# Kernel optimization log

Hardware: AMD Instinct MI355X
Metric: run time of the kernel (lower is better)

The kernel has to match this reference:

```python
import jax, jax.numpy as jnp
import numpy as np

SEQ, D_IN, D_OUT = 4096, 1024, 1024


def setup_inputs() -> dict:
    key = jax.random.key(0)
    k_emb, k_q, k_k, k_v = jax.random.split(key, 4)
    # torch Linear stores weight as [out, in]; we keep [in, out] for x @ W
    scale = 1.0 / np.sqrt(D_IN)
    return {
        "embeddings": jax.random.normal(k_emb, (SEQ, D_IN), dtype=jnp.float32),
        "w_query": jax.random.uniform(k_q, (D_IN, D_OUT), dtype=jnp.float32, minval=-scale, maxval=scale),
        "w_key": jax.random.uniform(k_k, (D_IN, D_OUT), dtype=jnp.float32, minval=-scale, maxval=scale),
        "w_value": jax.random.uniform(k_v, (D_IN, D_OUT), dtype=jnp.float32, minval=-scale, maxval=scale),
    }


def reference(embeddings, w_query, w_key, w_value):
    # QKV projections (bias=False)
    q = embeddings @ w_query  # [S, D_out]
    k = embeddings @ w_key    # [S, D_out]
    v = embeddings @ w_value  # [S, D_out]
    inv_sqrt_d = 1.0 / jnp.sqrt(jnp.asarray(k.shape[-1], dtype=q.dtype))
    scores = jnp.einsum("sd,td->st", q, k) * inv_sqrt_d  # [S, S]
    weights = jax.nn.softmax(scores, axis=-1)
    return weights @ v  # [S, D_out]
```

## Files before the change

kernel.cpp:

```cpp
#include <hip/hip_runtime.h>
#include <hip/hip_bf16.h>

typedef unsigned short u16;
typedef __bf16 bf16x8 __attribute__((ext_vector_type(8)));
typedef float f32x4 __attribute__((ext_vector_type(4)));
typedef unsigned short u16x8 __attribute__((ext_vector_type(8)));
typedef unsigned short u16x4 __attribute__((ext_vector_type(4)));

__device__ __forceinline__ float bf2f(u16 u) {
  unsigned x = ((unsigned)u) << 16;
  return __builtin_bit_cast(float, x);
}
__device__ __forceinline__ u16 f2bf(float f) {
  unsigned u = __builtin_bit_cast(unsigned, f);
  u += 0x7fffu + ((u >> 16) & 1u);
  return (u16)(u >> 16);
}

__device__ __forceinline__ void gload16(const u16* g, u16* lds) {
  __builtin_amdgcn_global_load_lds(
      (const __attribute__((address_space(1))) void*)g,
      (__attribute__((address_space(3))) void*)lds,
      16, 0, 0);
}

__device__ __forceinline__ void bar() {
  __builtin_amdgcn_sched_barrier(0);
  __builtin_amdgcn_s_barrier();
  __builtin_amdgcn_sched_barrier(0);
}
template <int N> __device__ __forceinline__ void wait_vm() {
  asm volatile("s_waitcnt vmcnt(%0)" :: "n"(N) : "memory");
  __builtin_amdgcn_sched_barrier(0);
}
__device__ __forceinline__ void wait_lgkm0() {
  asm volatile("s_waitcnt lgkmcnt(0)" ::: "memory");
  __builtin_amdgcn_sched_barrier(0);
}

#define OFF_A(d,h) (((d)*2+(h))*8192)
#define OFF_B(d,h) (32768 + ((d)*2+(h))*8192)

struct G256 {
  const u16 *gA0, *gA1, *gB0, *gB1;
  int dst0, dst1;
  int aoff0[4], aoff1[4], boff[4];
  u16* lds;
};

__device__ __forceinline__ int swz_slot(int row, int q) {
  return row * 4 + (q ^ ((row ^ (row >> 2)) & 3));
}

template <int W0, int W1, bool S0, bool S1>
__device__ __forceinline__ void ktile256(const G256& g, int s, f32x4 (&acc)[8][4]) {
  const int d = s & 1;
  const int kN1 = (s + 1) * 64 + 32;
  const int kN0 = (s + 2) * 64;
  bf16x8 af[8], bf[4];

#pragma unroll
  for (int i = 0; i < 4; ++i) af[i]     = *(const bf16x8*)(g.lds + OFF_A(d, 0) + g.aoff0[i]);
#pragma unroll
  for (int i = 0; i < 4; ++i) af[4 + i] = *(const bf16x8*)(g.lds + OFF_A(d, 0) + g.aoff1[i]);
#pragma unroll
  for (int j = 0; j < 4; ++j) bf[j]     = *(const bf16x8*)(g.lds + OFF_B(d, 0) + g.boff[j]);
  if (S0) {
    gload16(g.gA0 + kN1, g.lds + OFF_A(d ^ 1, 1) + g.dst0);
    gload16(g.gA1 + kN1, g.lds + OFF_A(d ^ 1, 1) + g.dst1);
    gload16(g.gB0 + kN1, g.lds + OFF_B(d ^ 1, 1) + g.dst0);
    gload16(g.gB1 + kN1, g.lds + OFF_B(d ^ 1, 1) + g.dst1);
  }
  wait_vm<W0>();
  bar();
  wait_lgkm0();
  __builtin_amdgcn_s_setprio(1);
#pragma unroll
  for (int i = 0; i < 8; ++i)
#pragma unroll
    for (int j = 0; j < 4; ++j)
      acc[i][j] = __builtin_amdgcn_mfma_f32_16x16x32_bf16(af[i], bf[j], acc[i][j], 0, 0, 0);
  __builtin_amdgcn_s_setprio(0);
  bar();

#pragma unroll
  for (int i = 0; i < 4; ++i) af[i]     = *(const bf16x8*)(g.lds + OFF_A(d, 1) + g.aoff0[i]);
#pragma unroll
  for (int i = 0; i < 4; ++i) af[4 + i] = *(const bf16x8*)(g.lds + OFF_A(d, 1) + g.aoff1[i]);
#pragma unroll
  for (int j = 0; j < 4; ++j) bf[j]     = *(const bf16x8*)(g.lds + OFF_B(d, 1) + g.boff[j]);
  if (S1) {
    gload16(g.gA0 + kN0, g.lds + OFF_A(d, 0) + g.dst0);
    gload16(g.gA1 + kN0, g.lds + OFF_A(d, 0) + g.dst1);
    gload16(g.gB0 + kN0, g.lds + OFF_B(d, 0) + g.dst0);
    gload16(g.gB1 + kN0, g.lds + OFF_B(d, 0) + g.dst1);
  }
  wait_vm<W1>();
  bar();
  wait_lgkm0();
  __builtin_amdgcn_s_setprio(1);
#pragma unroll
  for (int i = 0; i < 8; ++i)
#pragma unroll
    for (int j = 0; j < 4; ++j)
      acc[i][j] = __builtin_amdgcn_mfma_f32_16x16x32_bf16(af[i], bf[j], acc[i][j], 0, 0, 0);
  __builtin_amdgcn_s_setprio(0);
  bar();
}

template <int OUT_MODE, int NX, int NT>
__device__ __forceinline__ void gemm256_body(
    const u16* __restrict__ A, int lda, const u16* __restrict__ B, int ldb,
    void* __restrict__ C, int ldc, float cscale, u16* lds, int bid)
{
  static_assert(NT >= 3, "tail peel needs NT>=3");
  const int by = (bid & 7) + 8 * (bid / (8 * NX));
  const int bx = (bid >> 3) % NX;
  const int m0 = by * 256, n0 = bx * 256;
  const int t = threadIdx.x;
  const int w = t >> 6, l = t & 63;
  const int wm = (w >> 2) * 128, wn = (w & 3) * 64;
  const int fr = l & 15, q = l >> 4;

  G256 g;
  g.lds = lds;
  {
    const int s0 = w * 64 + l;
    const int r0 = s0 >> 2, r1 = r0 + 128;
    const int q0 = (s0 & 3) ^ ((r0 ^ (r0 >> 2)) & 3);
    const int q1 = (s0 & 3) ^ ((r1 ^ (r1 >> 2)) & 3);
    g.gA0 = A + (size_t)(m0 + r0) * lda + q0 * 8;
    g.gA1 = A + (size_t)(m0 + r1) * lda + q1 * 8;
    g.gB0 = B + (size_t)(n0 + r0) * ldb + q0 * 8;
    g.gB1 = B + (size_t)(n0 + r1) * ldb + q1 * 8;
    g.dst0 = (w * 64) * 8;
    g.dst1 = (512 + w * 64) * 8;
  }
#pragma unroll
  for (int i = 0; i < 4; ++i) {
    g.aoff0[i] = swz_slot(wm + 16 * i + fr, q) * 8;
    g.aoff1[i] = swz_slot(wm + 64 + 16 * i + fr, q) * 8;
    g.boff[i]  = swz_slot(wn + 16 * i + fr, q) * 8;
  }

  f32x4 acc[8][4] = {};

  gload16(g.gA0 + 0,  lds + OFF_A(0, 0) + g.dst0);
  gload16(g.gA1 + 0,  lds + OFF_A(0, 0) + g.dst1);
  gload16(g.gB0 + 0,  lds + OFF_B(0, 0) + g.dst0);
  gload16(g.gB1 + 0,  lds + OFF_B(0, 0) + g.dst1);
  gload16(g.gA0 + 32, lds + OFF_A(0, 1) + g.dst0);
  gload16(g.gA1 + 32, lds + OFF_A(0, 1) + g.dst1);
  gload16(g.gB0 + 32, lds + OFF_B(0, 1) + g.dst0);
  gload16(g.gB1 + 32, lds + OFF_B(0, 1) + g.dst1);
  gload16(g.gA0 + 64, lds + OFF_A(1, 0) + g.dst0);
  gload16(g.gA1 + 64, lds + OFF_A(1, 0) + g.dst1);
  gload16(g.gB0 + 64, lds + OFF_B(1, 0) + g.dst0);
  gload16(g.gB1 + 64, lds + OFF_B(1, 0) + g.dst1);
  wait_vm<8>();
  bar();

  for (int s = 0; s + 2 < NT; ++s)
    ktile256<8, 8, true, true>(g, s, acc);
  ktile256<8, 4, true, false>(g, NT - 2, acc);
  ktile256<0, 0, false, false>(g, NT - 1, acc);

  const int er = q * 4, ec = fr;
  const int rg = l >> 3, c = l & 7;

  if (OUT_MODE == 1) {
    u16* Ch = (u16*)C;
    u16* eb = lds + w * 4608;
#pragma unroll
    for (int half = 0; half < 2; ++half) {
#pragma unroll
      for (int i = 0; i < 4; ++i)
#pragma unroll
        for (int j = 0; j < 4; ++j)
#pragma unroll
          for (int r = 0; r < 4; ++r)
            eb[(16 * i + er + r) * 72 + 16 * j + ec] = f2bf(acc[4 * half + i][j][r] * cscale);
#pragma unroll
      for (int k = 0; k < 8; ++k) {
        const int row = k * 8 + rg;
        u16x8 v = *(const u16x8*)(eb + row * 72 + c * 8);
        *(u16x8*)(Ch + (size_t)(m0 + wm + 64 * half + row) * ldc + n0 + wn + c * 8) = v;
      }
    }
  } else {
    float* Cf = (float*)C;
    float* eb = (float*)lds + w * 2304;
#pragma unroll
    for (int half = 0; half < 2; ++half)
#pragma unroll
      for (int ip = 0; ip < 2; ++ip) {
#pragma unroll
        for (int ii = 0; ii < 2; ++ii)
#pragma unroll
          for (int j = 0; j < 4; ++j)
#pragma unroll
            for (int r = 0; r < 4; ++r)
              eb[(16 * ii + er + r) * 72 + 16 * j + ec] = acc[4 * half + 2 * ip + ii][j][r] * cscale;
#pragma unroll
        for (int k = 0; k < 4; ++k) {
          const int row = k * 8 + rg;
          float4 v0 = *(const float4*)(eb + row * 72 + c * 4);
          float4 v1 = *(const float4*)(eb + row * 72 + (c + 8) * 4);
          float* dst = Cf + (size_t)(m0 + wm + 64 * half + 32 * ip + row) * ldc + n0 + wn;
          *(float4*)(dst + c * 4) = v0;
          *(float4*)(dst + (c + 8) * 4) = v1;
        }
      }
  }
}

__global__ __launch_bounds__(512, 2) void gemm_qkv256(const u16* __restrict__ A,
                                                      const u16* __restrict__ B,
                                                      u16* __restrict__ C) {
  __shared__ __align__(16) u16 lds[65536];
  gemm256_body<1, 12, 16>(A, 1024, B, 1024, C, 3072, 1.0f, lds, blockIdx.x);
}

__global__ __launch_bounds__(512, 2) void gemm_score256(const u16* __restrict__ QKV,
                                                        u16* __restrict__ S) {
  __shared__ __align__(16) u16 lds[65536];
  gemm256_body<1, 16, 16>(QKV, 3072, QKV + 1024, 3072, S, 4096, 0.03125f, lds, blockIdx.x);
}

__global__ __launch_bounds__(512, 2) void gemm_pv256f(const u16* __restrict__ S,
                                                      const u16* __restrict__ Vt,
                                                      float* __restrict__ P4) {
  __shared__ __align__(16) u16 lds[65536];
  const int b = blockIdx.x;
  const int sp = b >> 6;
  float* Cp = P4 + (size_t)sp * 4096 * 1024;
  gemm256_body<0, 4, 16>(S + sp * 1024, 4096, Vt + sp * 1024, 4096,
                         Cp, 1024, 1.0f, lds, b & 63);
}

__global__ __launch_bounds__(512, 2) void gemm_pv256h(const u16* __restrict__ S,
                                                      const u16* __restrict__ Vt,
                                                      u16* __restrict__ P4) {
  __shared__ __align__(16) u16 lds[65536];
  const int b = blockIdx.x;
  const int sp = b >> 6;
  u16* Cp = P4 + (size_t)sp * 4096 * 1024;
  gemm256_body<1, 4, 16>(S + sp * 1024, 4096, Vt + sp * 1024, 4096,
                         Cp, 1024, 1.0f, lds, b & 63);
}

__global__ __launch_bounds__(256) void reduce4f(const float* __restrict__ P4,
                                                float* __restrict__ O) {
  const size_t i = ((size_t)blockIdx.x * 256 + threadIdx.x) * 4;
  const size_t st = (size_t)4096 * 1024;
  float4 a = *(const float4*)(P4 + i);
  float4 b = *(const float4*)(P4 + st + i);
  float4 c = *(const float4*)(P4 + 2 * st + i);
  float4 d = *(const float4*)(P4 + 3 * st + i);
  float4 o;
  o.x = (a.x + b.x) + (c.x + d.x);
  o.y = (a.y + b.y) + (c.y + d.y);
  o.z = (a.z + b.z) + (c.z + d.z);
  o.w = (a.w + b.w) + (c.w + d.w);
  *(float4*)(O + i) = o;
}

__global__ __launch_bounds__(256) void reduce4h(const u16* __restrict__ P4,
                                                float* __restrict__ O) {
  const size_t i = ((size_t)blockIdx.x * 256 + threadIdx.x) * 4;
  const size_t st = (size_t)4096 * 1024;
  u16x4 a = *(const u16x4*)(P4 + i);
  u16x4 b = *(const u16x4*)(P4 + st + i);
  u16x4 c = *(const u16x4*)(P4 + 2 * st + i);
  u16x4 d = *(const u16x4*)(P4 + 3 * st + i);
  float4 o;
  o.x = (bf2f(a.x) + bf2f(b.x)) + (bf2f(c.x) + bf2f(d.x));
  o.y = (bf2f(a.y) + bf2f(b.y)) + (bf2f(c.y) + bf2f(d.y));
  o.z = (bf2f(a.z) + bf2f(b.z)) + (bf2f(c.z) + bf2f(d.z));
  o.w = (bf2f(a.w) + bf2f(b.w)) + (bf2f(c.w) + bf2f(d.w));
  *(float4*)(O + i) = o;
}

__global__ __launch_bounds__(256) void prep(
    const float* __restrict__ E,
    const float* __restrict__ w0, const float* __restrict__ w1,
    const float* __restrict__ w2,
    u16* __restrict__ Ebf, u16* __restrict__ Wt)
{
  int b = blockIdx.x;
  if (b < 4096) {
    const int i = (b * 256 + threadIdx.x) * 4;
    float4 f = *(const float4*)(E + i);
    u16x4 o;
    o.x = f2bf(f.x); o.y = f2bf(f.y); o.z = f2bf(f.z); o.w = f2bf(f.w);
    *(u16x4*)(Ebf + i) = o;
  } else {
    b -= 4096;
    const int which = b >> 10;
    const int tile = b & 1023;
    const float* in = (which == 0) ? w0 : (which == 1) ? w1 : w2;
    u16* o = Wt + (size_t)which * 1024 * 1024;
    const int c0 = (tile & 31) * 32, r0 = (tile >> 5) * 32;
    __shared__ u16 tl[32][33];
    const int tx = threadIdx.x & 31, ty0 = threadIdx.x >> 5;
#pragma unroll
    for (int k = 0; k < 4; ++k) {
      const int ty = ty0 + k * 8;
      tl[ty][tx] = f2bf(in[(size_t)(r0 + ty) * 1024 + c0 + tx]);
    }
    __syncthreads();
#pragma unroll
    for (int k = 0; k < 4; ++k) {
      const int ty = ty0 + k * 8;
      o[(size_t)(c0 + ty) * 1024 + r0 + tx] = tl[tx][ty];
    }
  }
}

__global__ __launch_bounds__(256) void softmax_tv(u16* __restrict__ S,
                                                  const u16* __restrict__ QKV,
                                                  u16* __restrict__ Vt) {
  __shared__ float red[8];
  __shared__ u16 tl[32][33];
  const int b = blockIdx.x;
  if (b < 4096) {
    const int N = 4096;
    u16* p = S + (size_t)b * N;
    const int t = threadIdx.x;
    u16x8 u0 = ((const u16x8*)p)[t * 2];
    u16x8 u1 = ((const u16x8*)p)[t * 2 + 1];
    float v[16];
#pragma unroll
    for (int i = 0; i < 8; ++i) v[i] = bf2f(u0[i]);
#pragma unroll
    for (int i = 0; i < 8; ++i) v[8 + i] = bf2f(u1[i]);

    float m = -1e30f;
#pragma unroll
    for (int i = 0; i < 16; ++i) m = fmaxf(m, v[i]);
#pragma unroll
    for (int off = 32; off; off >>= 1) m = fmaxf(m, __shfl_xor(m, off));
    if ((t & 63) == 0) red[t >> 6] = m;
    __syncthreads();
    m = fmaxf(fmaxf(red[0], red[1]), fmaxf(red[2], red[3]));

    float s = 0.f;
#pragma unroll
    for (int i = 0; i < 16; ++i) { v[i] = __expf(v[i] - m); s += v[i]; }
#pragma unroll
    for (int off = 32; off; off >>= 1) s += __shfl_xor(s, off);
    if ((t & 63) == 0) red[4 + (t >> 6)] = s;
    __syncthreads();
    s = (red[4] + red[5]) + (red[6] + red[7]);
    const float inv = 1.0f / s;

    u16x8 o0, o1;
#pragma unroll
    for (int i = 0; i < 8; ++i) o0[i] = f2bf(v[i] * inv);
#pragma unroll
    for (int i = 0; i < 8; ++i) o1[i] = f2bf(v[8 + i] * inv);
    ((u16x8*)p)[t * 2] = o0;
    ((u16x8*)p)[t * 2 + 1] = o1;
  } else {
    const int v = b - 4096;
    const int c0 = (v & 31) * 32;
    const int r0 = (v >> 5) * 32;
    const int tx = threadIdx.x & 31, ty0 = threadIdx.x >> 5;
    const u16* Vin = QKV + 2048;
#pragma unroll
    for (int k = 0; k < 4; ++k) {
      const int ty = ty0 + k * 8;
      tl[ty][tx] = Vin[(size_t)(r0 + ty) * 3072 + c0 + tx];
    }
    __syncthreads();
#pragma unroll
    for (int k = 0; k < 4; ++k) {
      const int ty = ty0 + k * 8;
      Vt[(size_t)(c0 + ty) * 4096 + r0 + tx] = tl[tx][ty];
    }
  }
}

extern "C" void kernel_launch(void* const* d_in, const int* in_sizes, int n_in,
                              void* d_out, int out_size, void* d_ws, size_t ws_size,
                              hipStream_t stream) {
  const float* E  = (const float*)d_in[0];
  const float* Wq = (const float*)d_in[1];
  const float* Wk = (const float*)d_in[2];
  const float* Wv = (const float*)d_in[3];
  float* Out = (float*)d_out;

  char* w = (char*)d_ws;
  u16* Ebf = (u16*)(w);
  u16* Wt  = (u16*)(w + (size_t)(8u << 20));
  u16* QKV = (u16*)(w + (size_t)(14u << 20));
  u16* Vt  = (u16*)(w + (size_t)(38u << 20));
  u16* S   = (u16*)(w + (size_t)(46u << 20));

  prep<<<7168, 256, 0, stream>>>(E, Wq, Wk, Wv, Ebf, Wt);

  gemm_qkv256<<<192, 512, 0, stream>>>(Ebf, Wt, QKV);

  gemm_score256<<<256, 512, 0, stream>>>(QKV, S);

  softmax_tv<<<8192, 256, 0, stream>>>(S, QKV, Vt);

  if (ws_size >= ((size_t)146u << 20)) {
    float* P4 = (float*)(w + ((size_t)78u << 20));
    gemm_pv256f<<<256, 512, 0, stream>>>(S, Vt, P4);
    reduce4f<<<4096, 256, 0, stream>>>(P4, Out);
  } else {
    u16* P4 = (u16*)w;
    gemm_pv256h<<<256, 512, 0, stream>>>(S, Vt, P4);
    reduce4h<<<4096, 256, 0, stream>>>(P4, Out);
  }
}
```

Before: 218.8 us.

## Shrink GEMM tiles to 128x256 with triple-buffered K=32 pipeline

Replaces the 256x256 GEMM tile and its double-buffered two-half K pipeline with a 128x256 tile using a three-stage rotating LDS buffer at K=32 granularity and one barrier per phase. LDS per block drops, so launch bounds allow four blocks per CU, and grid sizes double to 384/512. The aim is more parallelism and better CU coverage on a 256-CU part, at the cost of lower arithmetic intensity per tile (more global/LDS traffic for the B operand) and more barriers per unit of work.

After: 221.4 us. No clear change (+1.2%).

```diff
diff --git a/kernel.cpp b/kernel.cpp
--- a/kernel.cpp
+++ b/kernel.cpp
@@ -38,133 +38,97 @@
   __builtin_amdgcn_sched_barrier(0);
 }
 
-#define OFF_A(d,h) (((d)*2+(h))*8192)
-#define OFF_B(d,h) (32768 + ((d)*2+(h))*8192)
-
-struct G256 {
-  const u16 *gA0, *gA1, *gB0, *gB1;
+__device__ __forceinline__ int h4(int r) { return ((r >> 1) ^ (r >> 3)) & 3; }
+
+#define ABUF(p) ((p) * 4096)
+#define BBUF(p) (12288 + (p) * 8192)
+
+struct GS {
+  const u16 *gA, *gB0, *gB1;
   int dst0, dst1;
-  int aoff0[4], aoff1[4], boff[4];
+  int aoff[4], boff[4];
   u16* lds;
 };
 
-__device__ __forceinline__ int swz_slot(int row, int q) {
-  return row * 4 + (q ^ ((row ^ (row >> 2)) & 3));
-}
-
-template <int W0, int W1, bool S0, bool S1>
-__device__ __forceinline__ void ktile256(const G256& g, int s, f32x4 (&acc)[8][4]) {
-  const int d = s & 1;
-  const int kN1 = (s + 1) * 64 + 32;
-  const int kN0 = (s + 2) * 64;
-  bf16x8 af[8], bf[4];
-
-#pragma unroll
-  for (int i = 0; i < 4; ++i) af[i]     = *(const bf16x8*)(g.lds + OFF_A(d, 0) + g.aoff0[i]);
-#pragma unroll
-  for (int i = 0; i < 4; ++i) af[4 + i] = *(const bf16x8*)(g.lds + OFF_A(d, 0) + g.aoff1[i]);
-#pragma unroll
-  for (int j = 0; j < 4; ++j) bf[j]     = *(const bf16x8*)(g.lds + OFF_B(d, 0) + g.boff[j]);
-  if (S0) {
-    gload16(g.gA0 + kN1, g.lds + OFF_A(d ^ 1, 1) + g.dst0);
-    gload16(g.gA1 + kN1, g.lds + OFF_A(d ^ 1, 1) + g.dst1);
-    gload16(g.gB0 + kN1, g.lds + OFF_B(d ^ 1, 1) + g.dst0);
-    gload16(g.gB1 + kN1, g.lds + OFF_B(d ^ 1, 1) + g.dst1);
-  }
-  wait_vm<W0>();
+template <bool STG, int W>
+__device__ __forceinline__ void phase128(const GS& g, int s, int p, f32x4 (&acc)[4][4]) {
+  wait_vm<W>();
   bar();
+  bf16x8 a[4], b[4];
+#pragma unroll
+  for (int i = 0; i < 4; ++i) a[i] = *(const bf16x8*)(g.lds + ABUF(p) + g.aoff[i]);
+#pragma unroll
+  for (int j = 0; j < 4; ++j) b[j] = *(const bf16x8*)(g.lds + BBUF(p) + g.boff[j]);
+  if (STG) {
+    const int kt = (s + 2) * 32;
+    const int p2 = (p + 2) % 3;
+    gload16(g.gA + kt, g.lds + ABUF(p2) + g.dst0);
+    gload16(g.gB0 + kt, g.lds + BBUF(p2) + g.dst0);
+    gload16(g.gB1 + kt, g.lds + BBUF(p2) + g.dst1);
+  }
   wait_lgkm0();
   __builtin_amdgcn_s_setprio(1);
 #pragma unroll
-  for (int i = 0; i < 8; ++i)
+  for (int i = 0; i < 4; ++i)
 #pragma unroll
     for (int j = 0; j < 4; ++j)
-      acc[i][j] = __builtin_amdgcn_mfma_f32_16x16x32_bf16(af[i], bf[j], acc[i][j], 0, 0, 0);
+      acc[i][j] = __builtin_amdgcn_mfma_f32_16x16x32_bf16(a[i], b[j], acc[i][j], 0, 0, 0);
   __builtin_amdgcn_s_setprio(0);
-  bar();
-
-#pragma unroll
-  for (int i = 0; i < 4; ++i) af[i]     = *(const bf16x8*)(g.lds + OFF_A(d, 1) + g.aoff0[i]);
-#pragma unroll
-  for (int i = 0; i < 4; ++i) af[4 + i] = *(const bf16x8*)(g.lds + OFF_A(d, 1) + g.aoff1[i]);
-#pragma unroll
-  for (int j = 0; j < 4; ++j) bf[j]     = *(const bf16x8*)(g.lds + OFF_B(d, 1) + g.boff[j]);
-  if (S1) {
-    gload16(g.gA0 + kN0, g.lds + OFF_A(d, 0) + g.dst0);
-    gload16(g.gA1 + kN0, g.lds + OFF_A(d, 0) + g.dst1);
-    gload16(g.gB0 + kN0, g.lds + OFF_B(d, 0) + g.dst0);
-    gload16(g.gB1 + kN0, g.lds + OFF_B(d, 0) + g.dst1);
-  }
-  wait_vm<W1>();
-  bar();
-  wait_lgkm0();
-  __builtin_amdgcn_s_setprio(1);
-#pragma unroll
-  for (int i = 0; i < 8; ++i)
-#pragma unroll
-    for (int j = 0; j < 4; ++j)
-      acc[i][j] = __builtin_amdgcn_mfma_f32_16x16x32_bf16(af[i], bf[j], acc[i][j], 0, 0, 0);
-  __builtin_amdgcn_s_setprio(0);
-  bar();
 }
 
 template <int OUT_MODE, int NX, int NT>
-__device__ __forceinline__ void gemm256_body(
+__device__ __forceinline__ void gemm128x256(
     const u16* __restrict__ A, int lda, const u16* __restrict__ B, int ldb,
     void* __restrict__ C, int ldc, float cscale, u16* lds, int bid)
 {
-  static_assert(NT >= 3, "tail peel needs NT>=3");
+  static_assert(NT % 3 == 2 && NT >= 5, "phase schedule needs NT==2 mod 3");
   const int by = (bid & 7) + 8 * (bid / (8 * NX));
   const int bx = (bid >> 3) % NX;
-  const int m0 = by * 256, n0 = bx * 256;
+  const int m0 = by * 128, n0 = bx * 256;
   const int t = threadIdx.x;
   const int w = t >> 6, l = t & 63;
-  const int wm = (w >> 2) * 128, wn = (w & 3) * 64;
+  const int wm = (w >> 2) * 64, wn = (w & 3) * 64;
   const int fr = l & 15, q = l >> 4;
 
-  G256 g;
+  GS g;
   g.lds = lds;
   {
-    const int s0 = w * 64 + l;
-    const int r0 = s0 >> 2, r1 = r0 + 128;
-    const int q0 = (s0 & 3) ^ ((r0 ^ (r0 >> 2)) & 3);
-    const int q1 = (s0 & 3) ^ ((r1 ^ (r1 >> 2)) & 3);
-    g.gA0 = A + (size_t)(m0 + r0) * lda + q0 * 8;
-    g.gA1 = A + (size_t)(m0 + r1) * lda + q1 * 8;
-    g.gB0 = B + (size_t)(n0 + r0) * ldb + q0 * 8;
-    g.gB1 = B + (size_t)(n0 + r1) * ldb + q1 * 8;
-    g.dst0 = (w * 64) * 8;
-    g.dst1 = (512 + w * 64) * 8;
+    const int sA = w * 64 + l;
+    const int rA = sA >> 2, cA = sA & 3;
+    const int sB1 = 512 + sA;
+    const int rB1 = sB1 >> 2, cB1 = sB1 & 3;
+    g.gA  = A + (size_t)(m0 + rA) * lda + (cA ^ h4(rA)) * 8;
+    g.gB0 = B + (size_t)(n0 + rA) * ldb + (cA ^ h4(rA)) * 8;
+    g.gB1 = B + (size_t)(n0 + rB1) * ldb + (cB1 ^ h4(rB1)) * 8;
+    g.dst0 = sA * 8;
+    g.dst1 = sB1 * 8;
   }
 #pragma unroll
   for (int i = 0; i < 4; ++i) {
-    g.aoff0[i] = swz_slot(wm + 16 * i + fr, q) * 8;
-    g.aoff1[i] = swz_slot(wm + 64 + 16 * i + fr, q) * 8;
-    g.boff[i]  = swz_slot(wn + 16 * i + fr, q) * 8;
-  }
-
-  f32x4 acc[8][4] = {};
-
-  gload16(g.gA0 + 0,  lds + OFF_A(0, 0) + g.dst0);
-  gload16(g.gA1 + 0,  lds + OFF_A(0, 0) + g.dst1);
-  gload16(g.gB0 + 0,  lds + OFF_B(0, 0) + g.dst0);
-  gload16(g.gB1 + 0,  lds + OFF_B(0, 0) + g.dst1);
-  gload16(g.gA0 + 32, lds + OFF_A(0, 1) + g.dst0);
-  gload16(g.gA1 + 32, lds + OFF_A(0, 1) + g.dst1);
-  gload16(g.gB0 + 32, lds + OFF_B(0, 1) + g.dst0);
-  gload16(g.gB1 + 32, lds + OFF_B(0, 1) + g.dst1);
-  gload16(g.gA0 + 64, lds + OFF_A(1, 0) + g.dst0);
-  gload16(g.gA1 + 64, lds + OFF_A(1, 0) + g.dst1);
-  gload16(g.gB0 + 64, lds + OFF_B(1, 0) + g.dst0);
-  gload16(g.gB1 + 64, lds + OFF_B(1, 0) + g.dst1);
-  wait_vm<8>();
+    const int ra = wm + 16 * i + fr;
+    const int rb = wn + 16 * i + fr;
+    g.aoff[i] = ra * 32 + (q ^ h4(ra)) * 8;
+    g.boff[i] = rb * 32 + (q ^ h4(rb)) * 8;
+  }
+
+  f32x4 acc[4][4] = {};
+
+  gload16(g.gA + 0,  lds + ABUF(0) + g.dst0);
+  gload16(g.gB0 + 0, lds + BBUF(0) + g.dst0);
+  gload16(g.gB1 + 0, lds + BBUF(0) + g.dst1);
+  gload16(g.gA + 32,  lds + ABUF(1) + g.dst0);
+  gload16(g.gB0 + 32, lds + BBUF(1) + g.dst0);
+  gload16(g.gB1 + 32, lds + BBUF(1) + g.dst1);
+
+  for (int s = 0; s < NT - 2; s += 3) {
+    phase128<true, 3>(g, s, 0, acc);
+    phase128<true, 3>(g, s + 1, 1, acc);
+    phase128<true, 3>(g, s + 2, 2, acc);
+  }
+  phase128<false, 3>(g, NT - 2, (NT - 2) % 3, acc);
+  phase128<false, 0>(g, NT - 1, (NT - 1) % 3, acc);
+
   bar();
-
-  for (int s = 0; s + 2 < NT; ++s)
-    ktile256<8, 8, true, true>(g, s, acc);
-  ktile256<8, 4, true, false>(g, NT - 2, acc);
-  ktile256<0, 0, false, false>(g, NT - 1, acc);
-
   const int er = q * 4, ec = fr;
   const int rg = l >> 3, c = l & 7;
 
@@ -172,81 +136,77 @@
     u16* Ch = (u16*)C;
     u16* eb = lds + w * 4608;
 #pragma unroll
-    for (int half = 0; half < 2; ++half) {
-#pragma unroll
-      for (int i = 0; i < 4; ++i)
-#pragma unroll
-        for (int j = 0; j < 4; ++j)
-#pragma unroll
-          for (int r = 0; r < 4; ++r)
-            eb[(16 * i + er + r) * 72 + 16 * j + ec] = f2bf(acc[4 * half + i][j][r] * cscale);
-#pragma unroll
-      for (int k = 0; k < 8; ++k) {
-        const int row = k * 8 + rg;
-        u16x8 v = *(const u16x8*)(eb + row * 72 + c * 8);
-        *(u16x8*)(Ch + (size_t)(m0 + wm + 64 * half + row) * ldc + n0 + wn + c * 8) = v;
-      }
+    for (int i = 0; i < 4; ++i)
+#pragma unroll
+      for (int j = 0; j < 4; ++j)
+#pragma unroll
+        for (int r = 0; r < 4; ++r)
+          eb[(16 * i + er + r) * 72 + 16 * j + ec] = f2bf(acc[i][j][r] * cscale);
+#pragma unroll
+    for (int k = 0; k < 8; ++k) {
+      const int row = k * 8 + rg;
+      u16x8 v = *(const u16x8*)(eb + row * 72 + c * 8);
+      *(u16x8*)(Ch + (size_t)(m0 + wm + row) * ldc + n0 + wn + c * 8) = v;
     }
   } else {
     float* Cf = (float*)C;
     float* eb = (float*)lds + w * 2304;
 #pragma unroll
-    for (int half = 0; half < 2; ++half)
-#pragma unroll
-      for (int ip = 0; ip < 2; ++ip) {
-#pragma unroll
-        for (int ii = 0; ii < 2; ++ii)
-#pragma unroll
-          for (int j = 0; j < 4; ++j)
-#pragma unroll
-            for (int r = 0; r < 4; ++r)
-              eb[(16 * ii + er + r) * 72 + 16 * j + ec] = acc[4 * half + 2 * ip + ii][j][r] * cscale;
-#pragma unroll
-        for (int k = 0; k < 4; ++k) {
-          const int row = k * 8 + rg;
-          float4 v0 = *(const float4*)(eb + row * 72 + c * 4);
-          float4 v1 = *(const float4*)(eb + row * 72 + (c + 8) * 4);
-          float* dst = Cf + (size_t)(m0 + wm + 64 * half + 32 * ip + row) * ldc + n0 + wn;
-          *(float4*)(dst + c * 4) = v0;
-          *(float4*)(dst + (c + 8) * 4) = v1;
-        }
+    for (int half = 0; half < 2; ++half) {
+#pragma unroll
+      for (int ii = 0; ii < 2; ++ii)
+#pragma unroll
+        for (int j = 0; j < 4; ++j)
+#pragma unroll
+          for (int r = 0; r < 4; ++r)
+            eb[(16 * ii + er + r) * 72 + 16 * j + ec] = acc[2 * half + ii][j][r] * cscale;
+#pragma unroll
+      for (int k = 0; k < 4; ++k) {
+        const int row = k * 8 + rg;
+        float4 v0 = *(const float4*)(eb + row * 72 + c * 4);
+        float4 v1 = *(const float4*)(eb + row * 72 + (c + 8) * 4);
+        float* dst = Cf + (size_t)(m0 + wm + 32 * half + row) * ldc + n0 + wn;
+        *(float4*)(dst + c * 4) = v0;
+        *(float4*)(dst + (c + 8) * 4) = v1;
       }
-  }
-}
-
-__global__ __launch_bounds__(512, 2) void gemm_qkv256(const u16* __restrict__ A,
+      if (half == 0) bar();
+    }
+  }
+}
+
+__global__ __launch_bounds__(512, 4) void gemm_qkv128(const u16* __restrict__ A,
                                                       const u16* __restrict__ B,
                                                       u16* __restrict__ C) {
-  __shared__ __align__(16) u16 lds[65536];
-  gemm256_body<1, 12, 16>(A, 1024, B, 1024, C, 3072, 1.0f, lds, blockIdx.x);
-}
-
-__global__ __launch_bounds__(512, 2) void gemm_score256(const u16* __restrict__ QKV,
+  __shared__ __align__(16) u16 lds[36864];
+  gemm128x256<1, 12, 32>(A, 1024, B, 1024, C, 3072, 1.0f, lds, blockIdx.x);
+}
+
+__global__ __launch_bounds__(512, 4) void gemm_score128(const u16* __restrict__ QKV,
                                                         u16* __restrict__ S) {
-  __shared__ __align__(16) u16 lds[65536];
-  gemm256_body<1, 16, 16>(QKV, 3072, QKV + 1024, 3072, S, 4096, 0.03125f, lds, blockIdx.x);
-}
-
-__global__ __launch_bounds__(512, 2) void gemm_pv256f(const u16* __restrict__ S,
+  __shared__ __align__(16) u16 lds[36864];
+  gemm128x256<1, 16, 32>(QKV, 3072, QKV + 1024, 3072, S, 4096, 0.03125f, lds, blockIdx.x);
+}
+
+__global__ __launch_bounds__(512, 4) void gemm_pv128f(const u16* __restrict__ S,
                                                       const u16* __restrict__ Vt,
                                                       float* __restrict__ P4) {
-  __shared__ __align__(16) u16 lds[65536];
+  __shared__ __align__(16) u16 lds[36864];
   const int b = blockIdx.x;
-  const int sp = b >> 6;
+  const int sp = b >> 7;
   float* Cp = P4 + (size_t)sp * 4096 * 1024;
-  gemm256_body<0, 4, 16>(S + sp * 1024, 4096, Vt + sp * 1024, 4096,
-                         Cp, 1024, 1.0f, lds, b & 63);
-}
-
-__global__ __launch_bounds__(512, 2) void gemm_pv256h(const u16* __restrict__ S,
+  gemm128x256<0, 4, 32>(S + sp * 1024, 4096, Vt + sp * 1024, 4096,
+                        Cp, 1024, 1.0f, lds, b & 127);
+}
+
+__global__ __launch_bounds__(512, 4) void gemm_pv128h(const u16* __restrict__ S,
                                                       const u16* __restrict__ Vt,
                                                       u16* __restrict__ P4) {
-  __shared__ __align__(16) u16 lds[65536];
+  __shared__ __align__(16) u16 lds[36864];
   const int b = blockIdx.x;
-  const int sp = b >> 6;
+  const int sp = b >> 7;
   u16* Cp = P4 + (size_t)sp * 4096 * 1024;
-  gemm256_body<1, 4, 16>(S + sp * 1024, 4096, Vt + sp * 1024, 4096,
-                         Cp, 1024, 1.0f, lds, b & 63);
+  gemm128x256<1, 4, 32>(S + sp * 1024, 4096, Vt + sp * 1024, 4096,
+                        Cp, 1024, 1.0f, lds, b & 127);
 }
 
 __global__ __launch_bounds__(256) void reduce4f(const float* __restrict__ P4,
@@ -399,19 +359,19 @@
 
   prep<<<7168, 256, 0, stream>>>(E, Wq, Wk, Wv, Ebf, Wt);
 
-  gemm_qkv256<<<192, 512, 0, stream>>>(Ebf, Wt, QKV);
-
-  gemm_score256<<<256, 512, 0, stream>>>(QKV, S);
+  gemm_qkv128<<<384, 512, 0, stream>>>(Ebf, Wt, QKV);
+
+  gemm_score128<<<512, 512, 0, stream>>>(QKV, S);
 
   softmax_tv<<<8192, 256, 0, stream>>>(S, QKV, Vt);
 
   if (ws_size >= ((size_t)146u << 20)) {
     float* P4 = (float*)(w + ((size_t)78u << 20));
-    gemm_pv256f<<<256, 512, 0, stream>>>(S, Vt, P4);
+    gemm_pv128f<<<512, 512, 0, stream>>>(S, Vt, P4);
     reduce4f<<<4096, 256, 0, stream>>>(P4, Out);
   } else {
     u16* P4 = (u16*)w;
-    gemm_pv256h<<<256, 512, 0, stream>>>(S, Vt, P4);
+    gemm_pv128h<<<512, 512, 0, stream>>>(S, Vt, P4);
     reduce4h<<<4096, 256, 0, stream>>>(P4, Out);
   }
 }
```

## Restructure GEMM k-loop to whole-tile staging with staggered half order per wave group

Applied to the files above, without the earlier changes.

The 256x256 GEMM main loop changes from a half-tile (32-wide k) staggered prefetch with two barriers per half to one wait and barrier per 64-wide k tile. The next tile is then issued in full after the compute barrier. Waves 0-3 process the k halves in order 0,1 while waves 4-7 use 1,0, so the two groups read different LDS regions at the same moment and spread LDS bank pressure. This removes a barrier pair per tile. The cost is a shallower prefetch window, since loads for tile s+2 are issued only after tile s is fully consumed.

New measurement: 280.6 us. +28.3%, slower.

```diff
diff --git a/kernel.cpp b/kernel.cpp
--- a/kernel.cpp
+++ b/kernel.cpp
@@ -52,60 +52,50 @@
   return row * 4 + (q ^ ((row ^ (row >> 2)) & 3));
 }
 
-template <int W0, int W1, bool S0, bool S1>
-__device__ __forceinline__ void ktile256(const G256& g, int s, f32x4 (&acc)[8][4]) {
-  const int d = s & 1;
-  const int kN1 = (s + 1) * 64 + 32;
-  const int kN0 = (s + 2) * 64;
-  bf16x8 af[8], bf[4];
-
-#pragma unroll
-  for (int i = 0; i < 4; ++i) af[i]     = *(const bf16x8*)(g.lds + OFF_A(d, 0) + g.aoff0[i]);
-#pragma unroll
-  for (int i = 0; i < 4; ++i) af[4 + i] = *(const bf16x8*)(g.lds + OFF_A(d, 0) + g.aoff1[i]);
-#pragma unroll
-  for (int j = 0; j < 4; ++j) bf[j]     = *(const bf16x8*)(g.lds + OFF_B(d, 0) + g.boff[j]);
-  if (S0) {
-    gload16(g.gA0 + kN1, g.lds + OFF_A(d ^ 1, 1) + g.dst0);
-    gload16(g.gA1 + kN1, g.lds + OFF_A(d ^ 1, 1) + g.dst1);
-    gload16(g.gB0 + kN1, g.lds + OFF_B(d ^ 1, 1) + g.dst0);
-    gload16(g.gB1 + kN1, g.lds + OFF_B(d ^ 1, 1) + g.dst1);
-  }
-  wait_vm<W0>();
-  bar();
+__device__ __forceinline__ void half_mfma(const G256& g, int d, int h, f32x4 (&acc)[8][4]) {
+  bf16x8 a[8], b[4];
+  const int oa = OFF_A(d, h), ob = OFF_B(d, h);
+#pragma unroll
+  for (int i = 0; i < 4; ++i) {
+    a[i]     = *(const bf16x8*)(g.lds + oa + g.aoff0[i]);
+    a[4 + i] = *(const bf16x8*)(g.lds + oa + g.aoff1[i]);
+  }
+#pragma unroll
+  for (int j = 0; j < 4; ++j) b[j] = *(const bf16x8*)(g.lds + ob + g.boff[j]);
   wait_lgkm0();
   __builtin_amdgcn_s_setprio(1);
 #pragma unroll
   for (int i = 0; i < 8; ++i)
 #pragma unroll
     for (int j = 0; j < 4; ++j)
-      acc[i][j] = __builtin_amdgcn_mfma_f32_16x16x32_bf16(af[i], bf[j], acc[i][j], 0, 0, 0);
+      acc[i][j] = __builtin_amdgcn_mfma_f32_16x16x32_bf16(a[i], b[j], acc[i][j], 0, 0, 0);
   __builtin_amdgcn_s_setprio(0);
+}
+
+template <int W, bool STG>
+__device__ __forceinline__ void ktile256(const G256& g, int s, bool lowgrp, f32x4 (&acc)[8][4]) {
+  const int d = s & 1;
+  wait_vm<W>();
   bar();
-
-#pragma unroll
-  for (int i = 0; i < 4; ++i) af[i]     = *(const bf16x8*)(g.lds + OFF_A(d, 1) + g.aoff0[i]);
-#pragma unroll
-  for (int i = 0; i < 4; ++i) af[4 + i] = *(const bf16x8*)(g.lds + OFF_A(d, 1) + g.aoff1[i]);
-#pragma unroll
-  for (int j = 0; j < 4; ++j) bf[j]     = *(const bf16x8*)(g.lds + OFF_B(d, 1) + g.boff[j]);
-  if (S1) {
-    gload16(g.gA0 + kN0, g.lds + OFF_A(d, 0) + g.dst0);
-    gload16(g.gA1 + kN0, g.lds + OFF_A(d, 0) + g.dst1);
-    gload16(g.gB0 + kN0, g.lds + OFF_B(d, 0) + g.dst0);
-    gload16(g.gB1 + kN0, g.lds + OFF_B(d, 0) + g.dst1);
-  }
-  wait_vm<W1>();
+  if (lowgrp) {
+    half_mfma(g, d, 0, acc);
+    half_mfma(g, d, 1, acc);
+  } else {
+    half_mfma(g, d, 1, acc);
+    half_mfma(g, d, 0, acc);
+  }
   bar();
-  wait_lgkm0();
-  __builtin_amdgcn_s_setprio(1);
-#pragma unroll
-  for (int i = 0; i < 8; ++i)
-#pragma unroll
-    for (int j = 0; j < 4; ++j)
-      acc[i][j] = __builtin_amdgcn_mfma_f32_16x16x32_bf16(af[i], bf[j], acc[i][j], 0, 0, 0);
-  __builtin_amdgcn_s_setprio(0);
-  bar();
+  if (STG) {
+    const int kt = (s + 2) * 64;
+    gload16(g.gA0 + kt,      g.lds + OFF_A(d, 0) + g.dst0);
+    gload16(g.gA1 + kt,      g.lds + OFF_A(d, 0) + g.dst1);
+    gload16(g.gA0 + kt + 32, g.lds + OFF_A(d, 1) + g.dst0);
+    gload16(g.gA1 + kt + 32, g.lds + OFF_A(d, 1) + g.dst1);
+    gload16(g.gB0 + kt,      g.lds + OFF_B(d, 0) + g.dst0);
+    gload16(g.gB1 + kt,      g.lds + OFF_B(d, 0) + g.dst1);
+    gload16(g.gB0 + kt + 32, g.lds + OFF_B(d, 1) + g.dst0);
+    gload16(g.gB1 + kt + 32, g.lds + OFF_B(d, 1) + g.dst1);
+  }
 }
 
 template <int OUT_MODE, int NX, int NT>
@@ -119,6 +109,7 @@
   const int m0 = by * 256, n0 = bx * 256;
   const int t = threadIdx.x;
   const int w = t >> 6, l = t & 63;
+  const bool lowgrp = (w < 4);
   const int wm = (w >> 2) * 128, wn = (w & 3) * 64;
   const int fr = l & 15, q = l >> 4;
 
@@ -145,26 +136,25 @@
 
   f32x4 acc[8][4] = {};
 
-  gload16(g.gA0 + 0,  lds + OFF_A(0, 0) + g.dst0);
-  gload16(g.gA1 + 0,  lds + OFF_A(0, 0) + g.dst1);
-  gload16(g.gB0 + 0,  lds + OFF_B(0, 0) + g.dst0);
-  gload16(g.gB1 + 0,  lds + OFF_B(0, 0) + g.dst1);
-  gload16(g.gA0 + 32, lds + OFF_A(0, 1) + g.dst0);
-  gload16(g.gA1 + 32, lds + OFF_A(0, 1) + g.dst1);
-  gload16(g.gB0 + 32, lds + OFF_B(0, 1) + g.dst0);
-  gload16(g.gB1 + 32, lds + OFF_B(0, 1) + g.dst1);
-  gload16(g.gA0 + 64, lds + OFF_A(1, 0) + g.dst0);
-  gload16(g.gA1 + 64, lds + OFF_A(1, 0) + g.dst1);
-  gload16(g.gB0 + 64, lds + OFF_B(1, 0) + g.dst0);
-  gload16(g.gB1 + 64, lds + OFF_B(1, 0) + g.dst1);
-  wait_vm<8>();
+#pragma unroll
+  for (int s = 0; s < 2; ++s) {
+    const int kt = s * 64, d = s & 1;
+    gload16(g.gA0 + kt,      lds + OFF_A(d, 0) + g.dst0);
+    gload16(g.gA1 + kt,      lds + OFF_A(d, 0) + g.dst1);
+    gload16(g.gA0 + kt + 32, lds + OFF_A(d, 1) + g.dst0);
+    gload16(g.gA1 + kt + 32, lds + OFF_A(d, 1) + g.dst1);
+    gload16(g.gB0 + kt,      lds + OFF_B(d, 0) + g.dst0);
+    gload16(g.gB1 + kt,      lds + OFF_B(d, 0) + g.dst1);
+    gload16(g.gB0 + kt + 32, lds + OFF_B(d, 1) + g.dst0);
+    gload16(g.gB1 + kt + 32, lds + OFF_B(d, 1) + g.dst1);
+  }
+
+  for (int s = 0; s < NT - 2; ++s)
+    ktile256<8, true>(g, s, lowgrp, acc);
+  ktile256<8, false>(g, NT - 2, lowgrp, acc);
+  ktile256<0, false>(g, NT - 1, lowgrp, acc);
+
   bar();
-
-  for (int s = 0; s + 2 < NT; ++s)
-    ktile256<8, 8, true, true>(g, s, acc);
-  ktile256<8, 4, true, false>(g, NT - 2, acc);
-  ktile256<0, 0, false, false>(g, NT - 1, acc);
-
   const int er = q * 4, ec = fr;
   const int rg = l >> 3, c = l & 7;
 
```
